# Kernel optimization log

Hardware: AMD Instinct MI355X
Metric: run time of the kernel (lower is better)

The kernel has to match this reference:

```python
import jax, jax.numpy as jnp
import numpy as np

N = 8192
IN_F = 512
OUT_F = 64
NEG_INF = -9e15

def setup_inputs() -> dict:
    key = jax.random.key(0)
    k1, k2, k3, k4 = jax.random.split(key, 4)
    node_features = jax.random.normal(k1, (N, IN_F), dtype=jnp.float32)
    adjacency_matrix = jax.random.randint(k2, (N, N), 0, 2, dtype=jnp.int32)
    # Xavier-uniform-like init (gain 1.414), scale irrelevant for correctness
    w_bound = 1.414 * np.sqrt(6.0 / (IN_F + OUT_F))
    a_bound = 1.414 * np.sqrt(6.0 / (2 * OUT_F + 1))
    weight_matrix = jax.random.uniform(k3, (IN_F, OUT_F), minval=-w_bound, maxval=w_bound, dtype=jnp.float32)
    attention_vector = jax.random.uniform(k4, (2 * OUT_F, 1), minval=-a_bound, maxval=a_bound, dtype=jnp.float32)
    return {
        "node_features": node_features,
        "adjacency_matrix": adjacency_matrix,
        "weight_matrix": weight_matrix,
        "attention_vector": attention_vector,
    }

def reference(node_features, adjacency_matrix, weight_matrix, attention_vector):
    # h: [N, F] transformed features
    h = node_features @ weight_matrix
    # score[i, j] = h[i] . a_left + h[j] . a_right
    a_left = attention_vector[:OUT_F, 0]   # [F]
    a_right = attention_vector[OUT_F:, 0]  # [F]
    scores = (h @ a_left)[:, None] + (h @ a_right)[None, :]  # [N, N]
    # NOTE: source defines leaky_relu but never applies it in forward — faithful omission.
    masked = jnp.where(adjacency_matrix > 0, scores, NEG_INF)
    attn = jax.nn.softmax(masked, axis=1)  # [N, N]
    # dropout p=0 / inference: no-op
    out = attn @ h  # [N, F]
    return jax.nn.elu(out)  # concat=True path
```

## Files before the change

kernel.cpp:

```cpp
#include <hip/hip_runtime.h>
#include <hip/hip_bf16.h>
#include <cstdint>

#define NN      8192
#define OF      64
#define NPAD    80
#define HWROWS  80
#define KSPLIT  8
#define LDSTR   72

#define OFF_HW  0
#define OFF_P   1310720

typedef __attribute__((ext_vector_type(8))) short  s16x8;
typedef __attribute__((ext_vector_type(4))) float  f32x4;

__device__ __forceinline__ unsigned short f2bf(float f) {
  unsigned int u = __float_as_uint(f);
  unsigned int r = (u + 0x7FFFu + ((u >> 16) & 1u)) >> 16;
  return (unsigned short)r;
}

__global__ __launch_bounds__(256) void k1_hw(const float* __restrict__ X,
                                             const float* __restrict__ W,
                                             const float* __restrict__ att,
                                             unsigned short* __restrict__ HW) {
  __shared__ float xs[16 * 516];
  __shared__ float ws[64 * 68];
  int t = threadIdx.x;
  int rb = blockIdx.x * 16;

  {
    const float4* src = (const float4*)(X + (size_t)rb * 512);
#pragma unroll
    for (int s = 0; s < 8; ++s) {
      int lid = s * 256 + t;
      int row = lid >> 7, kseg = lid & 127;
      *(float4*)&xs[row * 516 + kseg * 4] = src[row * 128 + kseg];
    }
  }

  int row = t >> 4, tx = t & 15;
  float4 acc = {0.f, 0.f, 0.f, 0.f};
  for (int kc = 0; kc < 8; ++kc) {
    __syncthreads();
#pragma unroll
    for (int s = 0; s < 4; ++s) {
      int lid = s * 256 + t;
      int k = lid >> 4, cs = lid & 15;
      *(float4*)&ws[k * 68 + cs * 4] =
          *(const float4*)(W + (size_t)(kc * 64 + k) * 64 + cs * 4);
    }
    __syncthreads();
#pragma unroll 16
    for (int k = 0; k < 64; ++k) {
      float x = xs[row * 516 + kc * 64 + k];
      float4 w4 = *(const float4*)&ws[k * 68 + tx * 4];
      acc.x += x * w4.x; acc.y += x * w4.y;
      acc.z += x * w4.z; acc.w += x * w4.w;
    }
  }

  float v = acc.x * att[64 + tx * 4]     + acc.y * att[64 + tx * 4 + 1] +
            acc.z * att[64 + tx * 4 + 2] + acc.w * att[64 + tx * 4 + 3];
#pragma unroll
  for (int m = 8; m > 0; m >>= 1) v += __shfl_xor(v, m, 64);
  float e = expf(v);

  int j = rb + row;
  unsigned short* hw = HW + j;
  float hv[4] = {acc.x, acc.y, acc.z, acc.w};
#pragma unroll
  for (int c = 0; c < 4; ++c)
    hw[(size_t)(tx * 4 + c) * NN] = f2bf(e * hv[c]);
  if (tx == 0) hw[(size_t)64 * NN] = f2bf(e);
  else         hw[(size_t)(64 + tx) * NN] = 0;
}

__device__ __forceinline__ s16x8 cvt8(int4 a, int4 b) {
  union { unsigned u[4]; s16x8 v; } rr;
  rr.u[0] = (unsigned)(a.x | (a.y << 16)) * 0x3F80u;
  rr.u[1] = (unsigned)(a.z | (a.w << 16)) * 0x3F80u;
  rr.u[2] = (unsigned)(b.x | (b.y << 16)) * 0x3F80u;
  rr.u[3] = (unsigned)(b.z | (b.w << 16)) * 0x3F80u;
  return rr.v;
}

__global__ __launch_bounds__(256, 4) void k3_gat(const int* __restrict__ A,
                                                 const unsigned short* __restrict__ HW,
                                                 float* __restrict__ P) {
  __shared__ unsigned short tile[HWROWS * LDSTR];

  int t = threadIdx.x;
  int rowTile = blockIdx.x >> 3;
  int ksId    = blockIdx.x & 7;
  int lane = t & 63, w = t >> 6;
  int l15 = lane & 15, q = lane >> 4;
  int rowBase = rowTile * 64 + w * 16;

  const int* ar0 = A + (size_t)(rowBase + l15) * NN + ksId * (NN / KSPLIT) + q * 8;

  f32x4 acc[5];
#pragma unroll
  for (int tt = 0; tt < 5; ++tt) acc[tt] = 0.f;

  int nrow0 = t >> 3,           sg0 = t & 7;
  int nrow1 = (t + 256) >> 3,   sg1 = t & 7;
  int nrow2 = (t + 512) >> 3,   sg2 = t & 7;
  bool third = (t < 128);

  int kk = ksId * (NN / KSPLIT);
  for (int step = 0; step < (NN / KSPLIT) / 64; ++step, kk += 64) {
    uint4 sv0 = *(const uint4*)(HW + (size_t)nrow0 * NN + kk + sg0 * 8);
    uint4 sv1 = *(const uint4*)(HW + (size_t)nrow1 * NN + kk + sg1 * 8);
    uint4 sv2;
    if (third) sv2 = *(const uint4*)(HW + (size_t)nrow2 * NN + kk + sg2 * 8);

    int4 a00 = *(const int4*)(ar0);
    int4 a01 = *(const int4*)(ar0 + 4);
    int4 a02 = *(const int4*)(ar0 + 32);
    int4 a03 = *(const int4*)(ar0 + 36);
    ar0 += 64;

    *(uint4*)&tile[nrow0 * LDSTR + sg0 * 8] = sv0;
    *(uint4*)&tile[nrow1 * LDSTR + sg1 * 8] = sv1;
    if (third) *(uint4*)&tile[nrow2 * LDSTR + sg2 * 8] = sv2;

    s16x8 af[2];
    af[0] = cvt8(a00, a01);
    af[1] = cvt8(a02, a03);

    __syncthreads();

#pragma unroll
    for (int ks = 0; ks < 2; ++ks)
#pragma unroll
      for (int tt = 0; tt < 5; ++tt) {
        int boff = (tt * 16 + l15) * LDSTR + ks * 32 + q * 8;
        s16x8 b = *(const s16x8*)&tile[boff];
        acc[tt] = __builtin_amdgcn_mfma_f32_16x16x32_bf16(af[ks], b, acc[tt], 0, 0, 0);
      }
    __syncthreads();
  }

  float* Pp = P + (size_t)ksId * NN * NPAD;
  int rb = rowBase + q * 4;
#pragma unroll
  for (int tt = 0; tt < 5; ++tt) {
    int col = tt * 16 + l15;
#pragma unroll
    for (int rg = 0; rg < 4; ++rg)
      Pp[(size_t)(rb + rg) * NPAD + col] = acc[tt][rg];
  }
}

__global__ __launch_bounds__(256) void k4_fin(const float* __restrict__ P,
                                              float* __restrict__ out) {
  int g = blockIdx.x * 256 + threadIdx.x;
  int i = g >> 6, c = g & 63;
  float num = 0.f, S = 0.f;
#pragma unroll
  for (int ks = 0; ks < KSPLIT; ++ks) {
    const float* p = P + (size_t)ks * NN * NPAD + (size_t)i * NPAD;
    num += p[c];
    S   += p[64];
  }
  float x = num / S;
  out[g] = x > 0.f ? x : expm1f(x);
}

extern "C" void kernel_launch(void* const* d_in, const int* in_sizes, int n_in,
                              void* d_out, int out_size, void* d_ws, size_t ws_size,
                              hipStream_t stream) {
  const float* X  = (const float*)d_in[0];
  const int*   A  = (const int*)d_in[1];
  const float* W  = (const float*)d_in[2];
  const float* av = (const float*)d_in[3];
  float* out = (float*)d_out;

  char* ws = (char*)d_ws;
  unsigned short* HW = (unsigned short*)(ws + OFF_HW);
  float*          P  = (float*)(ws + OFF_P);

  k1_hw<<<NN / 16, 256, 0, stream>>>(X, W, av, HW);
  k3_gat<<<128 * KSPLIT, 256, 0, stream>>>(A, HW, P);
  k4_fin<<<(size_t)NN * OF / 256, 256, 0, stream>>>(P, out);
}
```

Baseline: 414.0 us.

## Fuse split-K reduction and ELU finalize into GAT kernel, load HW directly

The work split changes from 64-row tiles with an 8-way cross-block K split to 16-row blocks where the 4 waves each take a quarter of K. Partials are reduced through LDS and the normalize+ELU epilogue is fused, which removes the P workspace round trip and the third kernel launch. The B operand (HW) is now loaded straight from global memory into registers instead of being staged through a shared LDS tile with barriers. In exchange, each wave reloads HW with no cross-wave sharing, more global traffic goes to the L2 for HW, and occupancy drops to 2 blocks per SIMD.

```diff
diff --git a/kernel.cpp b/kernel.cpp
--- a/kernel.cpp
+++ b/kernel.cpp
@@ -4,13 +4,10 @@
 
 #define NN      8192
 #define OF      64
-#define NPAD    80
 #define HWROWS  80
-#define KSPLIT  8
-#define LDSTR   72
+#define RSTR    84
 
 #define OFF_HW  0
-#define OFF_P   1310720
 
 typedef __attribute__((ext_vector_type(8))) short  s16x8;
 typedef __attribute__((ext_vector_type(4))) float  f32x4;
@@ -86,87 +83,81 @@
   return rr.v;
 }
 
-__global__ __launch_bounds__(256, 4) void k3_gat(const int* __restrict__ A,
+__global__ __launch_bounds__(256, 2) void k3_gat(const int* __restrict__ A,
                                                  const unsigned short* __restrict__ HW,
-                                                 float* __restrict__ P) {
-  __shared__ unsigned short tile[HWROWS * LDSTR];
+                                                 float* __restrict__ out) {
+  __shared__ float red[4 * 16 * RSTR];
 
   int t = threadIdx.x;
-  int rowTile = blockIdx.x >> 3;
-  int ksId    = blockIdx.x & 7;
   int lane = t & 63, w = t >> 6;
   int l15 = lane & 15, q = lane >> 4;
-  int rowBase = rowTile * 64 + w * 16;
+  int rowBase = blockIdx.x * 16;
 
-  const int* ar0 = A + (size_t)(rowBase + l15) * NN + ksId * (NN / KSPLIT) + q * 8;
+  const int* ar = A + (size_t)(rowBase + l15) * NN + w * 2048 + q * 8;
+
+  const unsigned short* bp[5];
+#pragma unroll
+  for (int tt = 0; tt < 5; ++tt)
+    bp[tt] = HW + (size_t)(tt * 16 + l15) * NN + w * 2048 + q * 8;
 
   f32x4 acc[5];
 #pragma unroll
   for (int tt = 0; tt < 5; ++tt) acc[tt] = 0.f;
 
-  int nrow0 = t >> 3,           sg0 = t & 7;
-  int nrow1 = (t + 256) >> 3,   sg1 = t & 7;
-  int nrow2 = (t + 512) >> 3,   sg2 = t & 7;
-  bool third = (t < 128);
+#pragma unroll 2
+  for (int step = 0; step < 32; ++step) {
+    int4 a00 = *(const int4*)(ar);
+    int4 a01 = *(const int4*)(ar + 4);
+    int4 a02 = *(const int4*)(ar + 32);
+    int4 a03 = *(const int4*)(ar + 36);
+    ar += 64;
 
-  int kk = ksId * (NN / KSPLIT);
-  for (int step = 0; step < (NN / KSPLIT) / 64; ++step, kk += 64) {
-    uint4 sv0 = *(const uint4*)(HW + (size_t)nrow0 * NN + kk + sg0 * 8);
-    uint4 sv1 = *(const uint4*)(HW + (size_t)nrow1 * NN + kk + sg1 * 8);
-    uint4 sv2;
-    if (third) sv2 = *(const uint4*)(HW + (size_t)nrow2 * NN + kk + sg2 * 8);
+    s16x8 b0[5], b1[5];
+#pragma unroll
+    for (int tt = 0; tt < 5; ++tt) {
+      b0[tt] = *(const s16x8*)(bp[tt]);
+      b1[tt] = *(const s16x8*)(bp[tt] + 32);
+      bp[tt] += 64;
+    }
 
-    int4 a00 = *(const int4*)(ar0);
-    int4 a01 = *(const int4*)(ar0 + 4);
-    int4 a02 = *(const int4*)(ar0 + 32);
-    int4 a03 = *(const int4*)(ar0 + 36);
-    ar0 += 64;
-
-    *(uint4*)&tile[nrow0 * LDSTR + sg0 * 8] = sv0;
-    *(uint4*)&tile[nrow1 * LDSTR + sg1 * 8] = sv1;
-    if (third) *(uint4*)&tile[nrow2 * LDSTR + sg2 * 8] = sv2;
-
-    s16x8 af[2];
-    af[0] = cvt8(a00, a01);
-    af[1] = cvt8(a02, a03);
-
-    __syncthreads();
+    s16x8 af0 = cvt8(a00, a01);
+    s16x8 af1 = cvt8(a02, a03);
 
 #pragma unroll
-    for (int ks = 0; ks < 2; ++ks)
+    for (int tt = 0; tt < 5; ++tt)
+      acc[tt] = __builtin_amdgcn_mfma_f32_16x16x32_bf16(af0, b0[tt], acc[tt], 0, 0, 0);
 #pragma unroll
-      for (int tt = 0; tt < 5; ++tt) {
-        int boff = (tt * 16 + l15) * LDSTR + ks * 32 + q * 8;
-        s16x8 b = *(const s16x8*)&tile[boff];
-        acc[tt] = __builtin_amdgcn_mfma_f32_16x16x32_bf16(af[ks], b, acc[tt], 0, 0, 0);
-      }
-    __syncthreads();
+    for (int tt = 0; tt < 5; ++tt)
+      acc[tt] = __builtin_amdgcn_mfma_f32_16x16x32_bf16(af1, b1[tt], acc[tt], 0, 0, 0);
   }
 
-  float* Pp = P + (size_t)ksId * NN * NPAD;
-  int rb = rowBase + q * 4;
+  float* slab = red + w * 16 * RSTR;
 #pragma unroll
-  for (int tt = 0; tt < 5; ++tt) {
-    int col = tt * 16 + l15;
+  for (int tt = 0; tt < 5; ++tt)
 #pragma unroll
     for (int rg = 0; rg < 4; ++rg)
-      Pp[(size_t)(rb + rg) * NPAD + col] = acc[tt][rg];
+      slab[(q * 4 + rg) * RSTR + tt * 16 + l15] = acc[tt][rg];
+  __syncthreads();
+
+#pragma unroll
+  for (int s = 0; s < 5; ++s) {
+    int e = s * 256 + t;
+    int r = e / 80, c = e - r * 80;
+    float v = red[r * RSTR + c] + red[(16 + r) * RSTR + c] +
+              red[(32 + r) * RSTR + c] + red[(48 + r) * RSTR + c];
+    red[r * RSTR + c] = v;
   }
-}
+  __syncthreads();
 
-__global__ __launch_bounds__(256) void k4_fin(const float* __restrict__ P,
-                                              float* __restrict__ out) {
-  int g = blockIdx.x * 256 + threadIdx.x;
-  int i = g >> 6, c = g & 63;
-  float num = 0.f, S = 0.f;
 #pragma unroll
-  for (int ks = 0; ks < KSPLIT; ++ks) {
-    const float* p = P + (size_t)ks * NN * NPAD + (size_t)i * NPAD;
-    num += p[c];
-    S   += p[64];
+  for (int i = 0; i < 4; ++i) {
+    int g = i * 256 + t;
+    int r = g >> 6, c = g & 63;
+    float num = red[r * RSTR + c];
+    float S   = red[r * RSTR + 64];
+    float x = num / S;
+    out[(size_t)(rowBase + r) * OF + c] = x > 0.f ? x : expm1f(x);
   }
-  float x = num / S;
-  out[g] = x > 0.f ? x : expm1f(x);
 }
 
 extern "C" void kernel_launch(void* const* d_in, const int* in_sizes, int n_in,
@@ -180,9 +171,7 @@
 
   char* ws = (char*)d_ws;
   unsigned short* HW = (unsigned short*)(ws + OFF_HW);
-  float*          P  = (float*)(ws + OFF_P);
 
   k1_hw<<<NN / 16, 256, 0, stream>>>(X, W, av, HW);
-  k3_gat<<<128 * KSPLIT, 256, 0, stream>>>(A, HW, P);
-  k4_fin<<<(size_t)NN * OF / 256, 256, 0, stream>>>(P, out);
+  k3_gat<<<NN / 16, 256, 0, stream>>>(A, HW, out);
 }
```

New measurement: 447.3 us. +8.0%, slower.

## Stage full HW column slice in LDS once per block and stream adjacency rows

Applied to the files above, without the earlier changes.

The main GAT kernel now splits K into 16 chunks of 512 columns. Each block loads the whole 65-row bf16 HW slice for its chunk into LDS once, then loops over four 16-row M tiles per wave, with register double-buffering of the adjacency loads. The per-64-column LDS refill and the two barriers per step are gone, and the padding rows of HW no longer need zeroing because the extra row is masked in registers. The cost is a larger LDS footprint (about 66KB), which lowers occupancy to 2 blocks per CU, and a partial-sum buffer with 16 slices that the finalize kernel must reduce.

```diff
diff --git a/kernel.cpp b/kernel.cpp
--- a/kernel.cpp
+++ b/kernel.cpp
@@ -4,10 +4,11 @@
 
 #define NN      8192
 #define OF      64
-#define NPAD    80
-#define HWROWS  80
-#define KSPLIT  8
-#define LDSTR   72
+#define KC      16
+#define CW      512
+#define SLROWS  65
+#define SLSTR   520
+#define PSTR    65
 
 #define OFF_HW  0
 #define OFF_P   1310720
@@ -74,7 +75,6 @@
   for (int c = 0; c < 4; ++c)
     hw[(size_t)(tx * 4 + c) * NN] = f2bf(e * hv[c]);
   if (tx == 0) hw[(size_t)64 * NN] = f2bf(e);
-  else         hw[(size_t)(64 + tx) * NN] = 0;
 }
 
 __device__ __forceinline__ s16x8 cvt8(int4 a, int4 b) {
@@ -86,71 +86,88 @@
   return rr.v;
 }
 
-__global__ __launch_bounds__(256, 4) void k3_gat(const int* __restrict__ A,
+__global__ __launch_bounds__(256, 2) void k3_gat(const int* __restrict__ A,
                                                  const unsigned short* __restrict__ HW,
                                                  float* __restrict__ P) {
-  __shared__ unsigned short tile[HWROWS * LDSTR];
+  __shared__ unsigned short bt[SLROWS * SLSTR];
 
   int t = threadIdx.x;
-  int rowTile = blockIdx.x >> 3;
-  int ksId    = blockIdx.x & 7;
+  int kc = blockIdx.x & 15;
+  int mg = blockIdx.x >> 4;
   int lane = t & 63, w = t >> 6;
   int l15 = lane & 15, q = lane >> 4;
-  int rowBase = rowTile * 64 + w * 16;
-
-  const int* ar0 = A + (size_t)(rowBase + l15) * NN + ksId * (NN / KSPLIT) + q * 8;
-
-  f32x4 acc[5];
-#pragma unroll
-  for (int tt = 0; tt < 5; ++tt) acc[tt] = 0.f;
-
-  int nrow0 = t >> 3,           sg0 = t & 7;
-  int nrow1 = (t + 256) >> 3,   sg1 = t & 7;
-  int nrow2 = (t + 512) >> 3,   sg2 = t & 7;
-  bool third = (t < 128);
-
-  int kk = ksId * (NN / KSPLIT);
-  for (int step = 0; step < (NN / KSPLIT) / 64; ++step, kk += 64) {
-    uint4 sv0 = *(const uint4*)(HW + (size_t)nrow0 * NN + kk + sg0 * 8);
-    uint4 sv1 = *(const uint4*)(HW + (size_t)nrow1 * NN + kk + sg1 * 8);
-    uint4 sv2;
-    if (third) sv2 = *(const uint4*)(HW + (size_t)nrow2 * NN + kk + sg2 * 8);
-
-    int4 a00 = *(const int4*)(ar0);
-    int4 a01 = *(const int4*)(ar0 + 4);
-    int4 a02 = *(const int4*)(ar0 + 32);
-    int4 a03 = *(const int4*)(ar0 + 36);
-    ar0 += 64;
-
-    *(uint4*)&tile[nrow0 * LDSTR + sg0 * 8] = sv0;
-    *(uint4*)&tile[nrow1 * LDSTR + sg1 * 8] = sv1;
-    if (third) *(uint4*)&tile[nrow2 * LDSTR + sg2 * 8] = sv2;
-
-    s16x8 af[2];
-    af[0] = cvt8(a00, a01);
-    af[1] = cvt8(a02, a03);
-
-    __syncthreads();
-
-#pragma unroll
-    for (int ks = 0; ks < 2; ++ks)
-#pragma unroll
-      for (int tt = 0; tt < 5; ++tt) {
-        int boff = (tt * 16 + l15) * LDSTR + ks * 32 + q * 8;
-        s16x8 b = *(const s16x8*)&tile[boff];
-        acc[tt] = __builtin_amdgcn_mfma_f32_16x16x32_bf16(af[ks], b, acc[tt], 0, 0, 0);
+  int k0 = kc * CW;
+
+#pragma unroll
+  for (int i = 0; i < 16; ++i) {
+    int lid = i * 256 + t;
+    int row = lid >> 6, sg = lid & 63;
+    *(uint4*)&bt[row * SLSTR + sg * 8] =
+        *(const uint4*)(HW + (size_t)row * NN + k0 + sg * 8);
+  }
+  if (t < 64)
+    *(uint4*)&bt[64 * SLSTR + t * 8] =
+        *(const uint4*)(HW + (size_t)64 * NN + k0 + t * 8);
+  __syncthreads();
+
+  float* Pp = P + (size_t)kc * NN * PSTR;
+  const s16x8 zero8 = {0, 0, 0, 0, 0, 0, 0, 0};
+
+  for (int mt = 0; mt < 4; ++mt) {
+    int rowM = mg * 256 + w * 64 + mt * 16;
+    const int* ar = A + (size_t)(rowM + l15) * NN + k0 + q * 8;
+
+    f32x4 acc[5];
+#pragma unroll
+    for (int tt = 0; tt < 5; ++tt) acc[tt] = 0.f;
+
+    int4 c0 = *(const int4*)(ar);
+    int4 c1 = *(const int4*)(ar + 4);
+    int4 c2 = *(const int4*)(ar + 32);
+    int4 c3 = *(const int4*)(ar + 36);
+    ar += 64;
+
+#pragma unroll
+    for (int step = 0; step < 8; ++step) {
+      int4 n0, n1, n2, n3;
+      if (step != 7) {
+        n0 = *(const int4*)(ar);
+        n1 = *(const int4*)(ar + 4);
+        n2 = *(const int4*)(ar + 32);
+        n3 = *(const int4*)(ar + 36);
+        ar += 64;
       }
-    __syncthreads();
-  }
-
-  float* Pp = P + (size_t)ksId * NN * NPAD;
-  int rb = rowBase + q * 4;
-#pragma unroll
-  for (int tt = 0; tt < 5; ++tt) {
-    int col = tt * 16 + l15;
-#pragma unroll
-    for (int rg = 0; rg < 4; ++rg)
-      Pp[(size_t)(rb + rg) * NPAD + col] = acc[tt][rg];
+
+      s16x8 af0 = cvt8(c0, c1);
+      s16x8 af1 = cvt8(c2, c3);
+
+#pragma unroll
+      for (int ks = 0; ks < 2; ++ks) {
+        s16x8 af = ks ? af1 : af0;
+        int kb = step * 64 + ks * 32 + q * 8;
+#pragma unroll
+        for (int tt = 0; tt < 4; ++tt) {
+          s16x8 b = *(const s16x8*)&bt[(tt * 16 + l15) * SLSTR + kb];
+          acc[tt] = __builtin_amdgcn_mfma_f32_16x16x32_bf16(af, b, acc[tt], 0, 0, 0);
+        }
+        s16x8 b4 = *(const s16x8*)&bt[64 * SLSTR + kb];
+        b4 = (l15 == 0) ? b4 : zero8;
+        acc[4] = __builtin_amdgcn_mfma_f32_16x16x32_bf16(af, b4, acc[4], 0, 0, 0);
+      }
+
+      c0 = n0; c1 = n1; c2 = n2; c3 = n3;
+    }
+
+    int rb = rowM + q * 4;
+#pragma unroll
+    for (int tt = 0; tt < 4; ++tt)
+#pragma unroll
+      for (int rg = 0; rg < 4; ++rg)
+        Pp[(size_t)(rb + rg) * PSTR + tt * 16 + l15] = acc[tt][rg];
+    if (l15 == 0)
+#pragma unroll
+      for (int rg = 0; rg < 4; ++rg)
+        Pp[(size_t)(rb + rg) * PSTR + 64] = acc[4][rg];
   }
 }
 
@@ -160,8 +177,8 @@
   int i = g >> 6, c = g & 63;
   float num = 0.f, S = 0.f;
 #pragma unroll
-  for (int ks = 0; ks < KSPLIT; ++ks) {
-    const float* p = P + (size_t)ks * NN * NPAD + (size_t)i * NPAD;
+  for (int kc = 0; kc < KC; ++kc) {
+    const float* p = P + (size_t)kc * NN * PSTR + (size_t)i * PSTR;
     num += p[c];
     S   += p[64];
   }
@@ -183,6 +200,6 @@
   float*          P  = (float*)(ws + OFF_P);
 
   k1_hw<<<NN / 16, 256, 0, stream>>>(X, W, av, HW);
-  k3_gat<<<128 * KSPLIT, 256, 0, stream>>>(A, HW, P);
+  k3_gat<<<512, 256, 0, stream>>>(A, HW, P);
   k4_fin<<<(size_t)NN * OF / 256, 256, 0, stream>>>(P, out);
 }
```

Result: slower. 451.7 us (+9.1%).
